# Kernel optimization log

Hardware: AMD Instinct MI355X
Metric: run time of the kernel (lower is better)

The kernel has to match this reference:

```python
import jax, jax.numpy as jnp
import numpy as np

EPS = 1e-12

def _l2norm(v, axis):
    # matches torch F.normalize: divide by norm clamped to eps
    n = jnp.sqrt(jnp.sum(v * v, axis=axis, keepdims=True))
    return v / jnp.maximum(n, EPS)

def setup_inputs() -> dict:
    key = jax.random.key(0)
    k1, k2 = jax.random.split(key)
    B, C, S, D = 256, 1000, 4, 512
    x = jax.random.normal(k1, (B, D), dtype=jnp.float32)
    # xavier_uniform over [C, S, D]: fan_in = S*D? torch treats dims (S, D) pairwise; approximate with uniform bound
    bound = float(np.sqrt(6.0 / (S + D)))
    W = jax.random.uniform(k2, (C, S, D), dtype=jnp.float32, minval=-bound, maxval=bound)
    return {"x": x, "W": W}

def reference(x, W):
    xn = _l2norm(x, axis=1)            # [B, D]
    Wn = _l2norm(W, axis=2)            # [C, S, D]
    logits = jnp.einsum('bd,csd->bcs', xn, Wn)        # [B, C, S]
    x_proj = jnp.einsum('bcs,csd->bcd', logits, Wn)   # [B, C, D]
    x_proj = _l2norm(x_proj, axis=2)
    out = jnp.einsum('bd,bcd->bc', xn, x_proj)        # [B, C]
    return out
```

## Files before the change

### kernel.cpp

```cpp
#include <hip/hip_runtime.h>

#define B_ 256
#define C_ 1000
#define D_ 512

typedef __bf16 bf16x4 __attribute__((ext_vector_type(4)));
typedef __bf16 bf16x8 __attribute__((ext_vector_type(8)));
typedef float  f32x4  __attribute__((ext_vector_type(4)));

__device__ __forceinline__ bf16x8 cvt8(float4 a, float4 b) {
    bf16x8 r;
    r[0] = (__bf16)a.x; r[1] = (__bf16)a.y; r[2] = (__bf16)a.z; r[3] = (__bf16)a.w;
    r[4] = (__bf16)b.x; r[5] = (__bf16)b.y; r[6] = (__bf16)b.z; r[7] = (__bf16)b.w;
    return r;
}
__device__ __forceinline__ bf16x4 cvt4(float4 a) {
    bf16x4 r;
    r[0] = (__bf16)a.x; r[1] = (__bf16)a.y; r[2] = (__bf16)a.z; r[3] = (__bf16)a.w;
    return r;
}

__global__ __launch_bounds__(256, 2) void k_fused(const float* __restrict__ x,
                                                  const float* __restrict__ W,
                                                  float* __restrict__ out) {
    __shared__ __align__(16) char smem[64 * 272];
    int blk = blockIdx.x;
    int ct = blk >> 1;
    int bh = blk & 1;
    int t = threadIdx.x;
    int lane = t & 63, wv = t >> 6;
    int l15 = lane & 15, quad = lane >> 4;

    const float* wbase = W + ct * 16 * D_;
    #pragma unroll
    for (int p = 0; p < 8; p++) {
        int ch = t + 256 * p;
        int row = ch >> 7, pos = ch & 127;
        float4 v = *(const float4*)(wbase + row * D_ + pos * 4);
        int ks = pos >> 3, qd = (pos >> 1) & 3, off = (pos & 1) * 4;
        *(bf16x4*)(smem + (ks * 4 + qd) * 272 + row * 16 + off * 2) = cvt4(v);
    }
    __syncthreads();

    int bt0 = bh * 8 + wv * 2;
    int bt1 = bt0 + 1;
    const float* xr0 = x + (bt0 * 16 + l15) * D_ + quad * 8;
    const float* xr1 = x + (bt1 * 16 + l15) * D_ + quad * 8;
    const char* lp = smem + quad * 272 + l15 * 16;

    f32x4 acc0 = {0.f, 0.f, 0.f, 0.f};
    f32x4 acc1 = {0.f, 0.f, 0.f, 0.f};
    f32x4 accg = {0.f, 0.f, 0.f, 0.f};
    float sn0 = 0.f, sn1 = 0.f;
    #pragma unroll
    for (int ks = 0; ks < 16; ks++) {
        float4 a0 = *(const float4*)(xr0 + ks * 32);
        float4 c0 = *(const float4*)(xr0 + ks * 32 + 4);
        float4 a1 = *(const float4*)(xr1 + ks * 32);
        float4 c1 = *(const float4*)(xr1 + ks * 32 + 4);
        bf16x8 af = *(const bf16x8*)(lp + ks * 1088);
        bf16x8 b0 = cvt8(a0, c0);
        bf16x8 b1 = cvt8(a1, c1);
        sn0 += a0.x*a0.x + a0.y*a0.y + a0.z*a0.z + a0.w*a0.w
             + c0.x*c0.x + c0.y*c0.y + c0.z*c0.z + c0.w*c0.w;
        sn1 += a1.x*a1.x + a1.y*a1.y + a1.z*a1.z + a1.w*a1.w
             + c1.x*c1.x + c1.y*c1.y + c1.z*c1.z + c1.w*c1.w;
        acc0 = __builtin_amdgcn_mfma_f32_16x16x32_bf16(af, b0, acc0, 0, 0, 0);
        acc1 = __builtin_amdgcn_mfma_f32_16x16x32_bf16(af, b1, acc1, 0, 0, 0);
        accg = __builtin_amdgcn_mfma_f32_16x16x32_bf16(af, af, accg, 0, 0, 0);
    }

    sn0 += __shfl_xor(sn0, 16); sn0 += __shfl_xor(sn0, 32);
    sn1 += __shfl_xor(sn1, 16); sn1 += __shfl_xor(sn1, 32);
    float ivx0 = 1.0f / fmaxf(sqrtf(sn0), 1e-12f);
    float ivx1 = 1.0f / fmaxf(sqrtf(sn1), 1e-12f);

    float g[4][4];
    #pragma unroll
    for (int s = 0; s < 4; s++) {
        float v = accg[s];
        #pragma unroll
        for (int q = 0; q < 4; q++) g[s][q] = __shfl(v, 20 * quad + q);
    }
    float iv[4];
    #pragma unroll
    for (int s = 0; s < 4; s++) iv[s] = 1.0f / fmaxf(sqrtf(fmaxf(g[s][s], 0.f)), 1e-12f);

    #pragma unroll
    for (int sub = 0; sub < 2; sub++) {
        int bt = sub ? bt1 : bt0;
        f32x4 acc = sub ? acc1 : acc0;
        float ivx = sub ? ivx1 : ivx0;
        float l[4];
        #pragma unroll
        for (int s = 0; s < 4; s++) l[s] = acc[s] * ivx * iv[s];
        float num = l[0]*l[0] + l[1]*l[1] + l[2]*l[2] + l[3]*l[3];
        float den2 = 0.f;
        #pragma unroll
        for (int s = 0; s < 4; s++) {
            float r = 0.f;
            #pragma unroll
            for (int q = 0; q < 4; q++) r += g[s][q] * iv[q] * l[q];
            den2 += l[s] * iv[s] * r;
        }
        float den = fmaxf(sqrtf(fmaxf(den2, 0.f)), 1e-12f);
        float val = num / den;

        float4 o;
        o.x = __shfl(val, l15);
        o.y = __shfl(val, l15 + 16);
        o.z = __shfl(val, l15 + 32);
        o.w = __shfl(val, l15 + 48);
        if (quad == 0)
            *(float4*)(out + (bt * 16 + l15) * C_ + ct * 4) = o;
    }
}

extern "C" void kernel_launch(void* const* d_in, const int* in_sizes, int n_in,
                              void* d_out, int out_size, void* d_ws, size_t ws_size,
                              hipStream_t stream) {
    const float* x = (const float*)d_in[0];
    const float* W = (const float*)d_in[1];
    float* out = (float*)d_out;
    k_fused<<<500, 256, 0, stream>>>(x, W, out);
}
```

Before: 78.55 us.

## Stage x tiles cooperatively in LDS as bf16 and compute x norms via MFMA

Instead of each wave loading its own fp32 x rows straight from global memory in MFMA fragment order, the block now cooperatively loads 128 rows of x in four K-chunks with coalesced float4 loads, converts them to bf16 and stores them in LDS. Waves then read their B fragments from LDS. The x squared norms are now taken from the diagonal of an extra x·x MFMA per sub-tile rather than an fp32 VALU reduction. Occupancy hint rises to 3 blocks per CU. In exchange this adds two barriers per chunk and about 35 KB more LDS per block, and the x norms are now computed from bf16-rounded values.

```diff
diff --git a/kernel.cpp b/kernel.cpp
--- a/kernel.cpp
+++ b/kernel.cpp
@@ -8,22 +8,17 @@
 typedef __bf16 bf16x8 __attribute__((ext_vector_type(8)));
 typedef float  f32x4  __attribute__((ext_vector_type(4)));
 
-__device__ __forceinline__ bf16x8 cvt8(float4 a, float4 b) {
-    bf16x8 r;
-    r[0] = (__bf16)a.x; r[1] = (__bf16)a.y; r[2] = (__bf16)a.z; r[3] = (__bf16)a.w;
-    r[4] = (__bf16)b.x; r[5] = (__bf16)b.y; r[6] = (__bf16)b.z; r[7] = (__bf16)b.w;
-    return r;
-}
 __device__ __forceinline__ bf16x4 cvt4(float4 a) {
     bf16x4 r;
     r[0] = (__bf16)a.x; r[1] = (__bf16)a.y; r[2] = (__bf16)a.z; r[3] = (__bf16)a.w;
     return r;
 }
 
-__global__ __launch_bounds__(256, 2) void k_fused(const float* __restrict__ x,
+__global__ __launch_bounds__(256, 3) void k_fused(const float* __restrict__ x,
                                                   const float* __restrict__ W,
                                                   float* __restrict__ out) {
-    __shared__ __align__(16) char smem[64 * 272];
+    __shared__ __align__(16) char smW[64 * 272];
+    __shared__ __align__(16) char smX[128 * 272];
     int blk = blockIdx.x;
     int ct = blk >> 1;
     int bh = blk & 1;
@@ -38,42 +33,45 @@
         int row = ch >> 7, pos = ch & 127;
         float4 v = *(const float4*)(wbase + row * D_ + pos * 4);
         int ks = pos >> 3, qd = (pos >> 1) & 3, off = (pos & 1) * 4;
-        *(bf16x4*)(smem + (ks * 4 + qd) * 272 + row * 16 + off * 2) = cvt4(v);
-    }
-    __syncthreads();
-
-    int bt0 = bh * 8 + wv * 2;
-    int bt1 = bt0 + 1;
-    const float* xr0 = x + (bt0 * 16 + l15) * D_ + quad * 8;
-    const float* xr1 = x + (bt1 * 16 + l15) * D_ + quad * 8;
-    const char* lp = smem + quad * 272 + l15 * 16;
-
-    f32x4 acc0 = {0.f, 0.f, 0.f, 0.f};
-    f32x4 acc1 = {0.f, 0.f, 0.f, 0.f};
-    f32x4 accg = {0.f, 0.f, 0.f, 0.f};
-    float sn0 = 0.f, sn1 = 0.f;
-    #pragma unroll
-    for (int ks = 0; ks < 16; ks++) {
-        float4 a0 = *(const float4*)(xr0 + ks * 32);
-        float4 c0 = *(const float4*)(xr0 + ks * 32 + 4);
-        float4 a1 = *(const float4*)(xr1 + ks * 32);
-        float4 c1 = *(const float4*)(xr1 + ks * 32 + 4);
-        bf16x8 af = *(const bf16x8*)(lp + ks * 1088);
-        bf16x8 b0 = cvt8(a0, c0);
-        bf16x8 b1 = cvt8(a1, c1);
-        sn0 += a0.x*a0.x + a0.y*a0.y + a0.z*a0.z + a0.w*a0.w
-             + c0.x*c0.x + c0.y*c0.y + c0.z*c0.z + c0.w*c0.w;
-        sn1 += a1.x*a1.x + a1.y*a1.y + a1.z*a1.z + a1.w*a1.w
-             + c1.x*c1.x + c1.y*c1.y + c1.z*c1.z + c1.w*c1.w;
-        acc0 = __builtin_amdgcn_mfma_f32_16x16x32_bf16(af, b0, acc0, 0, 0, 0);
-        acc1 = __builtin_amdgcn_mfma_f32_16x16x32_bf16(af, b1, acc1, 0, 0, 0);
-        accg = __builtin_amdgcn_mfma_f32_16x16x32_bf16(af, af, accg, 0, 0, 0);
+        *(bf16x4*)(smW + (ks * 4 + qd) * 272 + row * 16 + off * 2) = cvt4(v);
     }
 
-    sn0 += __shfl_xor(sn0, 16); sn0 += __shfl_xor(sn0, 32);
-    sn1 += __shfl_xor(sn1, 16); sn1 += __shfl_xor(sn1, 32);
-    float ivx0 = 1.0f / fmaxf(sqrtf(sn0), 1e-12f);
-    float ivx1 = 1.0f / fmaxf(sqrtf(sn1), 1e-12f);
+    int bt0 = wv * 2, bt1 = bt0 + 1;
+    const char* lpw  = smW + quad * 272 + l15 * 16;
+    const char* lpx0 = smX + (bt0 * 16 + quad) * 272 + l15 * 16;
+    const char* lpx1 = smX + (bt1 * 16 + quad) * 272 + l15 * 16;
+    const float* xbase = x + bh * 128 * D_;
+
+    f32x4 acc0  = {0.f, 0.f, 0.f, 0.f};
+    f32x4 acc1  = {0.f, 0.f, 0.f, 0.f};
+    f32x4 accg  = {0.f, 0.f, 0.f, 0.f};
+    f32x4 accx0 = {0.f, 0.f, 0.f, 0.f};
+    f32x4 accx1 = {0.f, 0.f, 0.f, 0.f};
+
+    for (int kc = 0; kc < 4; kc++) {
+        __syncthreads();
+        #pragma unroll
+        for (int p = 0; p < 16; p++) {
+            int id = t + 256 * p;
+            int row = id >> 5, col = id & 31;
+            float4 v = *(const float4*)(xbase + row * D_ + kc * 128 + col * 4);
+            int ksl = col >> 3, qd = (col >> 1) & 3, off = (col & 1) * 4;
+            *(bf16x4*)(smX + ((row >> 4) * 16 + ksl * 4 + qd) * 272
+                           + (row & 15) * 16 + off * 2) = cvt4(v);
+        }
+        __syncthreads();
+        #pragma unroll
+        for (int ksl = 0; ksl < 4; ksl++) {
+            bf16x8 af = *(const bf16x8*)(lpw + (kc * 4 + ksl) * 1088);
+            bf16x8 b0 = *(const bf16x8*)(lpx0 + ksl * 1088);
+            bf16x8 b1 = *(const bf16x8*)(lpx1 + ksl * 1088);
+            acc0  = __builtin_amdgcn_mfma_f32_16x16x32_bf16(af, b0, acc0, 0, 0, 0);
+            acc1  = __builtin_amdgcn_mfma_f32_16x16x32_bf16(af, b1, acc1, 0, 0, 0);
+            accg  = __builtin_amdgcn_mfma_f32_16x16x32_bf16(af, af, accg, 0, 0, 0);
+            accx0 = __builtin_amdgcn_mfma_f32_16x16x32_bf16(b0, b0, accx0, 0, 0, 0);
+            accx1 = __builtin_amdgcn_mfma_f32_16x16x32_bf16(b1, b1, accx1, 0, 0, 0);
+        }
+    }
 
     float g[4][4];
     #pragma unroll
@@ -86,11 +84,20 @@
     #pragma unroll
     for (int s = 0; s < 4; s++) iv[s] = 1.0f / fmaxf(sqrtf(fmaxf(g[s][s], 0.f)), 1e-12f);
 
+    int r3 = l15 & 3;
+    int srcl = ((l15 >> 2) << 4) | l15;
+    float p0 = (r3 == 0) ? accx0[0] : (r3 == 1) ? accx0[1] : (r3 == 2) ? accx0[2] : accx0[3];
+    float p1 = (r3 == 0) ? accx1[0] : (r3 == 1) ? accx1[1] : (r3 == 2) ? accx1[2] : accx1[3];
+    float d0 = __shfl(p0, srcl);
+    float d1 = __shfl(p1, srcl);
+    float ivx0 = 1.0f / fmaxf(sqrtf(fmaxf(d0, 0.f)), 1e-12f);
+    float ivx1 = 1.0f / fmaxf(sqrtf(fmaxf(d1, 0.f)), 1e-12f);
+
     #pragma unroll
     for (int sub = 0; sub < 2; sub++) {
-        int bt = sub ? bt1 : bt0;
         f32x4 acc = sub ? acc1 : acc0;
         float ivx = sub ? ivx1 : ivx0;
+        int bt = bh * 8 + wv * 2 + sub;
         float l[4];
         #pragma unroll
         for (int s = 0; s < 4; s++) l[s] = acc[s] * ivx * iv[s];
```

Result: faster. 70.86 us (-9.8%).
